# Kernel optimization log

Measured on AMD Instinct MI355X. Metric: run time of the kernel, lower is better.

## Reference

```python
import jax, jax.numpy as jnp
import numpy as np

N, L, C, NHEAD = 4, 2048, 1024, 8
D = C // NHEAD
EPS_ATTN = 1e-6
EPS_LN = 1e-5


def _w(key, shape, scale=0.02):
    return jax.random.normal(key, shape, dtype=jnp.float32) * scale


def setup_inputs() -> dict:
    key = jax.random.key(0)
    ks = jax.random.split(key, 32)
    inp = {
        'depth_feat': jax.random.normal(ks[0], (N, L, C), dtype=jnp.float32),
        'context_feat': jax.random.normal(ks[1], (N, L, C), dtype=jnp.float32),
        'depth_pos': jax.random.normal(ks[2], (N, L, C), dtype=jnp.float32),
        # encoder params (weights stored [in, out]; y = x @ W)
        'e_wq': _w(ks[3], (C, C)), 'e_wk': _w(ks[4], (C, C)), 'e_wv': _w(ks[5], (C, C)),
        'e_wm': _w(ks[6], (C, C)),
        'e_w1': _w(ks[7], (C, 2 * C)), 'e_w2': _w(ks[8], (2 * C, C)),
        'e_g1': jnp.ones((C,), jnp.float32), 'e_b1': jnp.zeros((C,), jnp.float32),
        'e_g2': jnp.ones((C,), jnp.float32), 'e_b2': jnp.zeros((C,), jnp.float32),
        # decoder params
        'd_wq0': _w(ks[9], (C, C)), 'd_wk0': _w(ks[10], (C, C)), 'd_wv0': _w(ks[11], (C, C)),
        'd_wm0': _w(ks[12], (C, C)),
        'd_wq1': _w(ks[13], (C, C)), 'd_wk1': _w(ks[14], (C, C)), 'd_wv1': _w(ks[15], (C, C)),
        'd_wm1': _w(ks[16], (C, C)),
        'd_w1': _w(ks[17], (C, 2 * C)), 'd_w2': _w(ks[18], (2 * C, C)),
        'd_g0': jnp.ones((C,), jnp.float32), 'd_b0': jnp.zeros((C,), jnp.float32),
        'd_g1': jnp.ones((C,), jnp.float32), 'd_b1': jnp.zeros((C,), jnp.float32),
        'd_g2': jnp.ones((C,), jnp.float32), 'd_b2': jnp.zeros((C,), jnp.float32),
    }
    return inp


def layernorm(x, g, b):
    m = jnp.mean(x, axis=-1, keepdims=True)
    v = jnp.mean(jnp.square(x - m), axis=-1, keepdims=True)
    return (x - m) * jax.lax.rsqrt(v + EPS_LN) * g + b


def linear_attention(q, k, v):
    # q,k,v: [N, L, H, D]; elu+1 feature map, O(L) kernelized attention
    Q = jax.nn.elu(q) + 1.0
    K = jax.nn.elu(k) + 1.0
    vlen = v.shape[1]
    v = v / vlen
    KV = jnp.einsum('nshd,nshv->nhdv', K, v)                    # [N,H,D,D]
    Z = 1.0 / (jnp.einsum('nlhd,nhd->nlh', Q, K.sum(axis=1)) + EPS_ATTN)
    out = jnp.einsum('nlhd,nhdv,nlh->nlhv', Q, KV, Z) * vlen    # [N,L,H,D]
    return out


def heads(x):
    n, l, c = x.shape
    return x.reshape(n, l, NHEAD, D)


def encoder_layer(x, wq, wk, wv, wm, w1, w2, g1, b1, g2, b2):
    n, l, c = x.shape
    msg = linear_attention(heads(x @ wq), heads(x @ wk), heads(x @ wv))
    msg = msg.reshape(n, l, c) @ wm
    x = x + layernorm(msg, g1, b1)
    x = x + layernorm(jax.nn.relu(x @ w1) @ w2, g2, b2)
    return x


def decoder_layer(x, src, wq0, wk0, wv0, wm0, wq1, wk1, wv1, wm1, w1, w2, g0, b0, g1, b1, g2, b2):
    n, l, c = x.shape
    msg = linear_attention(heads(x @ wq0), heads(x @ wk0), heads(x @ wv0))
    msg = msg.reshape(n, l, c) @ wm0
    x = x + layernorm(msg, g0, b0)
    msg = linear_attention(heads(x @ wq1), heads(src @ wk1), heads(src @ wv1))
    msg = msg.reshape(n, l, c) @ wm1
    x = x + layernorm(msg, g1, b1)
    x = x + layernorm(jax.nn.relu(x @ w1) @ w2, g2, b2)
    return x


def reference(depth_feat, context_feat, depth_pos,
              e_wq, e_wk, e_wv, e_wm, e_w1, e_w2, e_g1, e_b1, e_g2, e_b2,
              d_wq0, d_wk0, d_wv0, d_wm0, d_wq1, d_wk1, d_wv1, d_wm1,
              d_w1, d_w2, d_g0, d_b0, d_g1, d_b1, d_g2, d_b2):
    ctx = context_feat + depth_pos
    ctx = encoder_layer(ctx, e_wq, e_wk, e_wv, e_wm, e_w1, e_w2, e_g1, e_b1, e_g2, e_b2)
    out = decoder_layer(depth_feat, ctx,
                        d_wq0, d_wk0, d_wv0, d_wm0,
                        d_wq1, d_wk1, d_wv1, d_wm1,
                        d_w1, d_w2, d_g0, d_b0, d_g1, d_b1, d_g2, d_b2)
    return out
```

## Files before the change

### kernel.cpp

```cpp
#include <hip/hip_runtime.h>
#include <cstdint>

#define N_B 4
#define L_S 2048
#define C_F 1024
#define H_N 8
#define D_H 128
#define M_T (N_B * L_S)

typedef __bf16 bf16;
typedef __bf16 bf16x4 __attribute__((ext_vector_type(4)));
typedef __bf16 bf16x8 __attribute__((ext_vector_type(8)));
typedef float f32x4 __attribute__((ext_vector_type(4)));

typedef __attribute__((address_space(1))) void gvoid_t;
typedef __attribute__((address_space(3))) void lvoid_t;

__device__ __forceinline__ void lds_cp16(void* lds, const void* g) {
    __builtin_amdgcn_global_load_lds((gvoid_t*)g, (lvoid_t*)lds, 16, 0, 0);
}

__device__ __forceinline__ float elup1(float x) {
    return x > 0.0f ? x + 1.0f : __expf(x);
}

__device__ __forceinline__ void load4f(const void* base, size_t e0, int isbf, float* o) {
    if (isbf) {
        bf16x4 v = *(const bf16x4*)((const bf16*)base + e0);
        o[0] = (float)v[0]; o[1] = (float)v[1]; o[2] = (float)v[2]; o[3] = (float)v[3];
    } else {
        float4 v = *(const float4*)((const float*)base + e0);
        o[0] = v.x; o[1] = v.y; o[2] = v.z; o[3] = v.w;
    }
}

__global__ void detect_dtype(const unsigned int* g1, int* flag) {
    if (threadIdx.x == 0 && blockIdx.x == 0)
        *flag = (g1[0] == 0x3F803F80u) ? 1 : 0;
}

__global__ __launch_bounds__(256) void transpose_any(
        const void* __restrict__ src, bf16* __restrict__ dst,
        int R, int Cc, const int* __restrict__ flagp) {
    const int isbf = *flagp;
    __shared__ bf16 tile[32][33];
    const int bx = blockIdx.x * 32;
    const int by = blockIdx.y * 32;
    const int tx = threadIdx.x & 31;
    const int ty = threadIdx.x >> 5;
#pragma unroll
    for (int i = 0; i < 32; i += 8) {
        size_t ix = (size_t)(by + ty + i) * Cc + bx + tx;
        float v = isbf ? (float)((const bf16*)src)[ix] : ((const float*)src)[ix];
        tile[ty + i][tx] = (bf16)v;
    }
    __syncthreads();
#pragma unroll
    for (int i = 0; i < 32; i += 8)
        dst[(size_t)(bx + ty + i) * R + by + tx] = tile[tx][ty + i];
}

struct TAll {
    const void* src[16];
    unsigned int dstoff[16];
    int R[16];
    int C[16];
    int tile0[17];
};

__global__ __launch_bounds__(256) void transpose_all(
        TAll p, bf16* __restrict__ twall, const int* __restrict__ flagp) {
    const int isbf = *flagp;
    int gid = blockIdx.x;
    int w = 0;
    while (gid >= p.tile0[w + 1]) ++w;
    const int local = gid - p.tile0[w];
    const int R = p.R[w], Cc = p.C[w];
    const int tilesx = Cc >> 5;
    const int bx = (local % tilesx) * 32;
    const int by = (local / tilesx) * 32;
    const void* src = p.src[w];
    bf16* dst = twall + p.dstoff[w];
    __shared__ bf16 tile[32][33];
    const int tx = threadIdx.x & 31;
    const int ty = threadIdx.x >> 5;
#pragma unroll
    for (int i = 0; i < 32; i += 8) {
        size_t ix = (size_t)(by + ty + i) * Cc + bx + tx;
        float v = isbf ? (float)((const bf16*)src)[ix] : ((const float*)src)[ix];
        tile[ty + i][tx] = (bf16)v;
    }
    __syncthreads();
#pragma unroll
    for (int i = 0; i < 32; i += 8)
        dst[(size_t)(bx + ty + i) * R + by + tx] = tile[tx][ty + i];
}

template <int ACT>
__global__ __launch_bounds__(256, 2) void gemm_bt(
        const bf16* __restrict__ A, const bf16* __restrict__ Bt,
        bf16* __restrict__ C, int M, int N, int K) {
    __shared__ bf16 sA[128 * 64];
    __shared__ bf16 sB[128 * 64];
    const int t = threadIdx.x;
    const int lane = t & 63;
    const int w = t >> 6;
    const int wm = (w >> 1) * 64, wn = (w & 1) * 64;
    const int lr = lane & 15, lq = lane >> 4;
    const int m0 = blockIdx.y * 128, n0 = blockIdx.x * 128;

    f32x4 acc[4][4] = {};

    for (int kt = 0; kt < K; kt += 64) {
        const bf16* Ag = A + (size_t)m0 * K + kt;
        const bf16* Bg = Bt + (size_t)n0 * K + kt;
#pragma unroll
        for (int i = 0; i < 4; ++i) {
            int ci = t + i * 256;
            int r = ci >> 3, c8 = (ci & 7) * 8;
            lds_cp16(&sA[ci * 8], Ag + (size_t)r * K + c8);
        }
#pragma unroll
        for (int i = 0; i < 4; ++i) {
            int ci = t + i * 256;
            int r = ci >> 3, c8 = (ci & 7) * 8;
            lds_cp16(&sB[ci * 8], Bg + (size_t)r * K + c8);
        }
        __syncthreads();
#pragma unroll
        for (int kk = 0; kk < 64; kk += 32) {
            bf16x8 af[4], bfr[4];
#pragma unroll
            for (int mi = 0; mi < 4; ++mi)
                af[mi] = *(const bf16x8*)&sA[(wm + mi * 16 + lr) * 64 + kk + lq * 8];
#pragma unroll
            for (int ni = 0; ni < 4; ++ni)
                bfr[ni] = *(const bf16x8*)&sB[(wn + ni * 16 + lr) * 64 + kk + lq * 8];
#pragma unroll
            for (int mi = 0; mi < 4; ++mi)
#pragma unroll
                for (int ni = 0; ni < 4; ++ni)
                    acc[mi][ni] = __builtin_amdgcn_mfma_f32_16x16x32_bf16(
                        af[mi], bfr[ni], acc[mi][ni], 0, 0, 0);
        }
        __syncthreads();
    }
#pragma unroll
    for (int mi = 0; mi < 4; ++mi)
#pragma unroll
        for (int ni = 0; ni < 4; ++ni)
#pragma unroll
            for (int r = 0; r < 4; ++r) {
                int row = m0 + wm + mi * 16 + lq * 4 + r;
                int col = n0 + wn + ni * 16 + lr;
                float v = acc[mi][ni][r];
                if (ACT == 1) v = fmaxf(v, 0.0f);
                if (ACT == 2) v = v > 0.0f ? v + 1.0f : __expf(v);
                C[(size_t)row * N + col] = (bf16)v;
            }
}

__global__ __launch_bounds__(256, 2) void attn_kv_mfma(
        const bf16* __restrict__ ktg, const bf16* __restrict__ vtg,
        bf16* __restrict__ KVp, float* __restrict__ KSp) {
    const int nh = blockIdx.x;
    const int chunk = blockIdx.y;
    const int n = nh >> 3, h = nh & 7;
    const int t = threadIdx.x;
    const int lane = t & 63;
    const int w = t >> 6;
    const int wm = (w >> 1) * 64, wn = (w & 1) * 64;
    const int lr = lane & 15, lq = lane >> 4;
    __shared__ bf16 sA[128 * 64];
    __shared__ bf16 sB[128 * 64];
    const size_t base = (size_t)(h * D_H) * M_T + (size_t)n * L_S + chunk * 128;

    f32x4 acc[4][4] = {};
    float ks = 0.0f;
    const int dh = t >> 1, half = (t & 1) * 32;

    for (int kt = 0; kt < 128; kt += 64) {
        const bf16* Ag = vtg + base + kt;
        const bf16* Bg = ktg + base + kt;
#pragma unroll
        for (int i = 0; i < 4; ++i) {
            int ci = t + i * 256;
            int r = ci >> 3, c8 = (ci & 7) * 8;
            lds_cp16(&sA[ci * 8], Ag + (size_t)r * M_T + c8);
        }
#pragma unroll
        for (int i = 0; i < 4; ++i) {
            int ci = t + i * 256;
            int r = ci >> 3, c8 = (ci & 7) * 8;
            lds_cp16(&sB[ci * 8], Bg + (size_t)r * M_T + c8);
        }
        __syncthreads();
#pragma unroll
        for (int j = 0; j < 4; ++j) {
            bf16x8 v = *(const bf16x8*)&sB[dh * 64 + half + j * 8];
#pragma unroll
            for (int m = 0; m < 8; ++m) ks += (float)v[m];
        }
#pragma unroll
        for (int kk = 0; kk < 64; kk += 32) {
            bf16x8 af[4], bfr[4];
#pragma unroll
            for (int mi = 0; mi < 4; ++mi)
                af[mi] = *(const bf16x8*)&sA[(wm + mi * 16 + lr) * 64 + kk + lq * 8];
#pragma unroll
            for (int ni = 0; ni < 4; ++ni)
                bfr[ni] = *(const bf16x8*)&sB[(wn + ni * 16 + lr) * 64 + kk + lq * 8];
#pragma unroll
            for (int mi = 0; mi < 4; ++mi)
#pragma unroll
                for (int ni = 0; ni < 4; ++ni)
                    acc[mi][ni] = __builtin_amdgcn_mfma_f32_16x16x32_bf16(
                        af[mi], bfr[ni], acc[mi][ni], 0, 0, 0);
        }
        __syncthreads();
    }
    float ko = __shfl_xor(ks, 1);
    if (!(t & 1)) KSp[(nh * 16 + chunk) * D_H + dh] = ks + ko;

    bf16* out = KVp + ((size_t)(nh * 16 + chunk)) * (D_H * D_H);
#pragma unroll
    for (int mi = 0; mi < 4; ++mi)
#pragma unroll
        for (int ni = 0; ni < 4; ++ni)
#pragma unroll
            for (int r = 0; r < 4; ++r) {
                int row = wm + mi * 16 + lq * 4 + r;
                int col = wn + ni * 16 + lr;
                out[(size_t)row * D_H + col] = (bf16)acc[mi][ni][r];
            }
}

__global__ __launch_bounds__(256) void attn_reduce_t(
        const bf16* __restrict__ KVp, const float* __restrict__ KSp,
        bf16* __restrict__ KVt, float* __restrict__ Ksum) {
    const int nh = blockIdx.x;
    const int es = blockIdx.y;
    const int t = threadIdx.x;
    const size_t base = (size_t)nh * 16 * (D_H * D_H) + es * 4096 + t * 16;
    float fa[16] = {};
    for (int c = 0; c < 16; ++c) {
        const bf16* p = KVp + base + (size_t)c * (D_H * D_H);
        bf16x8 a = *(const bf16x8*)p;
        bf16x8 b = *(const bf16x8*)(p + 8);
#pragma unroll
        for (int m = 0; m < 8; ++m) { fa[m] += (float)a[m]; fa[8 + m] += (float)b[m]; }
    }
    bf16* o = KVt + (size_t)nh * (D_H * D_H) + es * 4096 + t * 16;
    bf16x8 oa, ob;
#pragma unroll
    for (int m = 0; m < 8; ++m) { oa[m] = (bf16)fa[m]; ob[m] = (bf16)fa[8 + m]; }
    *(bf16x8*)o = oa;
    *(bf16x8*)(o + 8) = ob;
    if (es == 0 && t < 128) {
        float s = 0.0f;
#pragma unroll
        for (int c = 0; c < 16; ++c) s += KSp[(nh * 16 + c) * D_H + t];
        Ksum[nh * D_H + t] = s;
    }
}

__global__ __launch_bounds__(256, 2) void attn_out_mfma(
        const bf16* __restrict__ qb, const bf16* __restrict__ KVt,
        const float* __restrict__ Ksum, bf16* __restrict__ ab) {
    const int nh = blockIdx.x, tile = blockIdx.y;
    const int n = nh >> 3, h = nh & 7;
    const int t = threadIdx.x;
    const int lane = t & 63;
    const int w = t >> 6;
    const int wm = (w >> 1) * 64, wn = (w & 1) * 64;
    const int lr = lane & 15, lq = lane >> 4;
    __shared__ bf16 sA[128 * 64];
    __shared__ bf16 sB[128 * 64];
    __shared__ float sKs[128];
    __shared__ float sZp[128][2];
    __shared__ float sZ[128];
    if (t < 128) sKs[t] = Ksum[nh * D_H + t];

    f32x4 acc[4][4] = {};
    float zacc = 0.0f;
    const int zrow = t >> 1, zoff = (t & 1) * 32;
    const size_t qbase = ((size_t)(n * L_S + tile * 128)) * C_F + h * D_H;

    for (int kt = 0; kt < 128; kt += 64) {
        __syncthreads();
#pragma unroll
        for (int i = 0; i < 4; ++i) {
            int ci = t + i * 256;
            int r = ci >> 3, c8 = (ci & 7) * 8;
            lds_cp16(&sA[ci * 8], qb + qbase + (size_t)r * C_F + kt + c8);
            lds_cp16(&sB[ci * 8], KVt + (size_t)nh * (D_H * D_H) + (size_t)r * D_H + kt + c8);
        }
        __syncthreads();
#pragma unroll 8
        for (int j = 0; j < 32; ++j)
            zacc += (float)sA[zrow * 64 + zoff + j] * sKs[kt + zoff + j];
#pragma unroll
        for (int kk = 0; kk < 64; kk += 32) {
            bf16x8 af[4], bfr[4];
#pragma unroll
            for (int mi = 0; mi < 4; ++mi)
                af[mi] = *(const bf16x8*)&sA[(wm + mi * 16 + lr) * 64 + kk + lq * 8];
#pragma unroll
            for (int ni = 0; ni < 4; ++ni)
                bfr[ni] = *(const bf16x8*)&sB[(wn + ni * 16 + lr) * 64 + kk + lq * 8];
#pragma unroll
            for (int mi = 0; mi < 4; ++mi)
#pragma unroll
                for (int ni = 0; ni < 4; ++ni)
                    acc[mi][ni] = __builtin_amdgcn_mfma_f32_16x16x32_bf16(
                        af[mi], bfr[ni], acc[mi][ni], 0, 0, 0);
        }
    }
    sZp[zrow][t & 1] = zacc;
    __syncthreads();
    if (t < 128) sZ[t] = 1.0f / (sZp[t][0] + sZp[t][1] + 1e-6f);
    __syncthreads();
#pragma unroll
    for (int mi = 0; mi < 4; ++mi)
#pragma unroll
        for (int ni = 0; ni < 4; ++ni)
#pragma unroll
            for (int r = 0; r < 4; ++r) {
                int row = wm + mi * 16 + lq * 4 + r;
                int col = wn + ni * 16 + lr;
                ab[qbase + (size_t)row * C_F + col] = (bf16)(acc[mi][ni][r] * sZ[row]);
            }
}

template <int F32OUT>
__global__ __launch_bounds__(256) void ln_res(
        const bf16* __restrict__ msg, const void* __restrict__ g,
        const void* __restrict__ bb, const int* __restrict__ flagp,
        const bf16* __restrict__ xin, void* __restrict__ xout) {
    const int isbf = *flagp;
    const int row = blockIdx.x * 4 + (threadIdx.x >> 6);
    const int lane = threadIdx.x & 63;
    const size_t base = (size_t)row * C_F;
    float m[16];
#pragma unroll
    for (int k = 0; k < 4; ++k) {
        bf16x4 v = *(const bf16x4*)(msg + base + k * 256 + lane * 4);
        m[k * 4 + 0] = (float)v[0]; m[k * 4 + 1] = (float)v[1];
        m[k * 4 + 2] = (float)v[2]; m[k * 4 + 3] = (float)v[3];
    }
    float s1 = 0.0f, s2 = 0.0f;
#pragma unroll
    for (int q = 0; q < 16; ++q) { s1 += m[q]; s2 += m[q] * m[q]; }
#pragma unroll
    for (int off = 32; off > 0; off >>= 1) {
        s1 += __shfl_down(s1, off);
        s2 += __shfl_down(s2, off);
    }
    s1 = __shfl(s1, 0);
    s2 = __shfl(s2, 0);
    const float mean = s1 / C_F;
    const float rs = rsqrtf(s2 / C_F - mean * mean + 1e-5f);
#pragma unroll
    for (int k = 0; k < 4; ++k) {
        const size_t cix = k * 256 + lane * 4;
        float ga[4], ba[4];
        load4f(g, cix, isbf, ga);
        load4f(bb, cix, isbf, ba);
        bf16x4 x4 = *(const bf16x4*)(xin + base + cix);
        if (F32OUT) {
            float4 of;
            of.x = (float)x4[0] + (m[k * 4 + 0] - mean) * rs * ga[0] + ba[0];
            of.y = (float)x4[1] + (m[k * 4 + 1] - mean) * rs * ga[1] + ba[1];
            of.z = (float)x4[2] + (m[k * 4 + 2] - mean) * rs * ga[2] + ba[2];
            of.w = (float)x4[3] + (m[k * 4 + 3] - mean) * rs * ga[3] + ba[3];
            *(float4*)((float*)xout + base + cix) = of;
        } else {
            bf16x4 ob;
            ob[0] = (bf16)((float)x4[0] + (m[k * 4 + 0] - mean) * rs * ga[0] + ba[0]);
            ob[1] = (bf16)((float)x4[1] + (m[k * 4 + 1] - mean) * rs * ga[1] + ba[1]);
            ob[2] = (bf16)((float)x4[2] + (m[k * 4 + 2] - mean) * rs * ga[2] + ba[2]);
            ob[3] = (bf16)((float)x4[3] + (m[k * 4 + 3] - mean) * rs * ga[3] + ba[3]);
            *(bf16x4*)((bf16*)xout + base + cix) = ob;
        }
    }
}

__global__ __launch_bounds__(256) void init_ctx_kernel(
        const void* __restrict__ a, const void* __restrict__ b,
        const int* __restrict__ flagp, bf16* __restrict__ xb) {
    const int isbf = *flagp;
    const size_t i = ((size_t)blockIdx.x * 256 + threadIdx.x) * 4;
    float av[4], bv[4];
    load4f(a, i, isbf, av);
    load4f(b, i, isbf, bv);
    bf16x4 o;
#pragma unroll
    for (int q = 0; q < 4; ++q) o[q] = (bf16)(av[q] + bv[q]);
    *(bf16x4*)(xb + i) = o;
}

__global__ __launch_bounds__(256) void conv_copy_kernel(
        const void* __restrict__ a, const int* __restrict__ flagp,
        bf16* __restrict__ xb) {
    const int isbf = *flagp;
    const size_t i = ((size_t)blockIdx.x * 256 + threadIdx.x) * 4;
    float av[4];
    load4f(a, i, isbf, av);
    bf16x4 o;
#pragma unroll
    for (int q = 0; q < 4; ++q) o[q] = (bf16)av[q];
    *(bf16x4*)(xb + i) = o;
}

extern "C" void kernel_launch(void* const* d_in, const int* in_sizes, int n_in,
                              void* d_out, int out_size, void* d_ws, size_t ws_size,
                              hipStream_t stream) {
    const size_t MB = 1u << 20;
    uint8_t* W = (uint8_t*)d_ws;
    bf16* xb    = (bf16*)(W + 0);
    bf16* ctxb  = (bf16*)(W + 16 * MB);
    bf16* qb    = (bf16*)(W + 32 * MB);
    bf16* kb    = (bf16*)(W + 48 * MB);
    bf16* vb    = (bf16*)(W + 64 * MB);
    bf16* hb    = kb;
    bf16* S     = (bf16*)(W + 80 * MB);
    bf16* TW    = (bf16*)(W + 96 * MB);
    bf16* KVp   = S;
    float* KSp  = (float*)(W + 100 * MB);
    bf16* KVt   = (bf16*)(W + 101 * MB);
    float* Ksum = (float*)(W + 102 * MB);
    int*   flag = (int*)(W + 102 * MB + 64 * 1024);
    bf16* TWall = (bf16*)(W + 104 * MB);
    const bool batched = (ws_size >= 145 * MB);

    detect_dtype<<<1, 64, 0, stream>>>((const unsigned int*)d_in[9], flag);

    const int widx[16] = {3,4,5,6,7,8,13,14,15,16,17,18,19,20,21,22};
    const int wR[16]   = {1024,1024,1024,1024,1024,2048,1024,1024,1024,1024,
                          1024,1024,1024,1024,1024,2048};
    const int wC[16]   = {1024,1024,1024,1024,2048,1024,1024,1024,1024,1024,
                          1024,1024,1024,1024,2048,1024};
    unsigned int off[16];
    if (batched) {
        TAll p;
        unsigned int acc = 0;
        int tacc = 0;
        for (int i = 0; i < 16; ++i) {
            p.src[i] = d_in[widx[i]];
            p.dstoff[i] = acc;
            p.R[i] = wR[i];
            p.C[i] = wC[i];
            p.tile0[i] = tacc;
            off[i] = acc;
            acc += (unsigned int)wR[i] * wC[i];
            tacc += (wR[i] / 32) * (wC[i] / 32);
        }
        p.tile0[16] = tacc;
        transpose_all<<<tacc, 256, 0, stream>>>(p, TWall, flag);
    }
    auto BT = [&](int idx) -> const bf16* {
        int s = 0;
        for (int i = 0; i < 16; ++i) if (widx[i] == idx) { s = i; break; }
        if (batched) return TWall + off[s];
        dim3 g(wC[s] / 32, wR[s] / 32);
        transpose_any<<<g, 256, 0, stream>>>(d_in[idx], TW, wR[s], wC[s], flag);
        return TW;
    };
    auto TG = [&](int idx, const bf16* A, bf16* Cc, int Nn, int Kk, int act) {
        const bf16* Bt = BT(idx);
        dim3 g(Nn / 128, M_T / 128);
        if (act == 1)      gemm_bt<1><<<g, 256, 0, stream>>>(A, Bt, Cc, M_T, Nn, Kk);
        else if (act == 2) gemm_bt<2><<<g, 256, 0, stream>>>(A, Bt, Cc, M_T, Nn, Kk);
        else               gemm_bt<0><<<g, 256, 0, stream>>>(A, Bt, Cc, M_T, Nn, Kk);
    };
    auto TGT = [&](int idx, const bf16* X, bf16* Ct, int act) {
        const bf16* Wt = BT(idx);
        dim3 g(M_T / 128, C_F / 128);
        if (act == 2) gemm_bt<2><<<g, 256, 0, stream>>>(Wt, X, Ct, C_F, M_T, C_F);
        else          gemm_bt<0><<<g, 256, 0, stream>>>(Wt, X, Ct, C_F, M_T, C_F);
    };
    auto ATT = [&](const bf16* q, const bf16* k, const bf16* v, bf16* o) {
        attn_kv_mfma<<<dim3(32, 16), 256, 0, stream>>>(k, v, KVp, KSp);
        attn_reduce_t<<<dim3(32, 4), 256, 0, stream>>>(KVp, KSp, KVt, Ksum);
        attn_out_mfma<<<dim3(32, 16), 256, 0, stream>>>(q, KVt, Ksum, o);
    };
    auto LN = [&](const bf16* m, int gi, int bi, const bf16* xi, bf16* xo) {
        ln_res<0><<<M_T / 4, 256, 0, stream>>>(m, d_in[gi], d_in[bi], flag, xi, (void*)xo);
    };

    init_ctx_kernel<<<M_T * C_F / 1024, 256, 0, stream>>>(d_in[1], d_in[2], flag, xb);
    TG(3, xb, qb, C_F, C_F, 2);
    TGT(4, xb, kb, 2);
    TGT(5, xb, vb, 0);
    ATT(qb, kb, vb, S);
    TG(6, S, qb, C_F, C_F, 0);
    LN(qb, 9, 10, xb, xb);
    TG(7, xb, hb, 2 * C_F, C_F, 1);
    TG(8, hb, S, C_F, 2 * C_F, 0);
    LN(S, 11, 12, xb, ctxb);

    conv_copy_kernel<<<M_T * C_F / 1024, 256, 0, stream>>>(d_in[0], flag, xb);
    TG(13, xb, qb, C_F, C_F, 2);
    TGT(14, xb, kb, 2);
    TGT(15, xb, vb, 0);
    ATT(qb, kb, vb, S);
    TG(16, S, qb, C_F, C_F, 0);
    LN(qb, 23, 24, xb, xb);
    TG(17, xb, qb, C_F, C_F, 2);
    TGT(18, ctxb, kb, 2);
    TGT(19, ctxb, vb, 0);
    ATT(qb, kb, vb, S);
    TG(20, S, qb, C_F, C_F, 0);
    LN(qb, 25, 26, xb, xb);
    TG(21, xb, hb, 2 * C_F, C_F, 1);
    TG(22, hb, S, C_F, 2 * C_F, 0);
    ln_res<1><<<M_T / 4, 256, 0, stream>>>(S, d_in[27], d_in[28], flag, xb, d_out);
}
```

Measured before the change: 933.1 us.

## Add 256x256 pipelined GEMM and fuse K/V projections into one launch

```diff
diff --git a/kernel.cpp b/kernel.cpp
--- a/kernel.cpp
+++ b/kernel.cpp
@@ -156,6 +156,104 @@
                 float v = acc[mi][ni][r];
                 if (ACT == 1) v = fmaxf(v, 0.0f);
                 if (ACT == 2) v = v > 0.0f ? v + 1.0f : __expf(v);
+                C[(size_t)row * N + col] = (bf16)v;
+            }
+}
+
+#define STAGE_T(sarr, Gbase, ldstride, Tt)                                    \
+    {                                                                         \
+        const int sl_ = (Tt) & 3;                                             \
+        _Pragma("unroll")                                                     \
+        for (int i_ = 0; i_ < 2; ++i_) {                                      \
+            int ci_ = t + i_ * 512;                                           \
+            int r_ = ci_ >> 2, c8_ = (ci_ & 3) * 8;                           \
+            lds_cp16(&sarr[sl_ * 8192 + ci_ * 8],                             \
+                     (Gbase) + (size_t)r_ * (ldstride) + ((Tt) << 5) +        \
+                         (c8_ ^ ((r_ & 3) << 3)));                            \
+        }                                                                     \
+    }
+
+template <int ACT>
+__global__ __launch_bounds__(512, 2) void gemm256(
+        const bf16* __restrict__ A, const bf16* __restrict__ Bt,
+        bf16* __restrict__ C, int M, int N, int K, int actsplit) {
+    __shared__ bf16 sA[4 * 256 * 32];
+    __shared__ bf16 sB[4 * 256 * 32];
+    const int t = threadIdx.x;
+    const int lane = t & 63;
+    const int w = t >> 6;
+    const int wr = w >> 2, wc = w & 3;
+    const int lr = lane & 15, lq = lane >> 4;
+    const int m0 = blockIdx.y * 256, n0 = blockIdx.x * 256;
+    const int nt = K >> 5;
+
+    const bf16* Ab = A + (size_t)m0 * K;
+    const bf16* Bb = Bt + (size_t)n0 * K;
+
+    f32x4 acc[8][4] = {};
+
+    STAGE_T(sA, Ab, K, 0); STAGE_T(sB, Bb, K, 0);
+    STAGE_T(sA, Ab, K, 1); STAGE_T(sB, Bb, K, 1);
+    asm volatile("s_waitcnt vmcnt(4)" ::: "memory");
+    __builtin_amdgcn_s_barrier();
+
+    for (int T = 0; T < nt; ++T) {
+        const bf16* sAs = &sA[(T & 3) * 8192];
+        const bf16* sBs = &sB[(T & 3) * 8192];
+        bf16x8 af[4], bfr[4], ag[4];
+#pragma unroll
+        for (int mi = 0; mi < 4; ++mi) {
+            int row = wr * 128 + mi * 16 + lr;
+            af[mi] = *(const bf16x8*)&sAs[row * 32 + ((lq * 8) ^ ((row & 3) << 3))];
+        }
+#pragma unroll
+        for (int ni = 0; ni < 4; ++ni) {
+            int row = wc * 64 + ni * 16 + lr;
+            bfr[ni] = *(const bf16x8*)&sBs[row * 32 + ((lq * 8) ^ ((row & 3) << 3))];
+        }
+        if (T + 2 < nt) STAGE_T(sA, Ab, K, T + 2);
+        __builtin_amdgcn_s_barrier();
+        __builtin_amdgcn_s_setprio(1);
+#pragma unroll
+        for (int mi = 0; mi < 4; ++mi)
+#pragma unroll
+            for (int ni = 0; ni < 4; ++ni)
+                acc[mi][ni] = __builtin_amdgcn_mfma_f32_16x16x32_bf16(
+                    af[mi], bfr[ni], acc[mi][ni], 0, 0, 0);
+        __builtin_amdgcn_s_setprio(0);
+        __builtin_amdgcn_s_barrier();
+#pragma unroll
+        for (int mi = 0; mi < 4; ++mi) {
+            int row = wr * 128 + (mi + 4) * 16 + lr;
+            ag[mi] = *(const bf16x8*)&sAs[row * 32 + ((lq * 8) ^ ((row & 3) << 3))];
+        }
+        if (T + 2 < nt) STAGE_T(sB, Bb, K, T + 2);
+        __builtin_amdgcn_s_barrier();
+        __builtin_amdgcn_s_setprio(1);
+#pragma unroll
+        for (int mi = 0; mi < 4; ++mi)
+#pragma unroll
+            for (int ni = 0; ni < 4; ++ni)
+                acc[mi + 4][ni] = __builtin_amdgcn_mfma_f32_16x16x32_bf16(
+                    ag[mi], bfr[ni], acc[mi + 4][ni], 0, 0, 0);
+        __builtin_amdgcn_s_setprio(0);
+        if (T + 1 < nt) {
+            if (T + 2 < nt) asm volatile("s_waitcnt vmcnt(4)" ::: "memory");
+            else            asm volatile("s_waitcnt vmcnt(0)" ::: "memory");
+        }
+        __builtin_amdgcn_s_barrier();
+    }
+#pragma unroll
+    for (int mi = 0; mi < 8; ++mi)
+#pragma unroll
+        for (int ni = 0; ni < 4; ++ni)
+#pragma unroll
+            for (int r = 0; r < 4; ++r) {
+                int row = m0 + wr * 128 + mi * 16 + lq * 4 + r;
+                int col = n0 + wc * 64 + ni * 16 + lr;
+                float v = acc[mi][ni][r];
+                if (ACT == 1) v = fmaxf(v, 0.0f);
+                if (ACT == 3 && row < actsplit) v = v > 0.0f ? v + 1.0f : __expf(v);
                 C[(size_t)row * N + col] = (bf16)v;
             }
 }
@@ -441,26 +539,30 @@
     const int wC[16]   = {1024,1024,1024,1024,2048,1024,1024,1024,1024,1024,
                           1024,1024,1024,1024,2048,1024};
     unsigned int off[16];
+    {
+        unsigned int acc = 0;
+        for (int i = 0; i < 16; ++i) { off[i] = acc; acc += (unsigned int)wR[i] * wC[i]; }
+    }
     if (batched) {
         TAll p;
-        unsigned int acc = 0;
         int tacc = 0;
         for (int i = 0; i < 16; ++i) {
             p.src[i] = d_in[widx[i]];
-            p.dstoff[i] = acc;
+            p.dstoff[i] = off[i];
             p.R[i] = wR[i];
             p.C[i] = wC[i];
             p.tile0[i] = tacc;
-            off[i] = acc;
-            acc += (unsigned int)wR[i] * wC[i];
             tacc += (wR[i] / 32) * (wC[i] / 32);
         }
         p.tile0[16] = tacc;
         transpose_all<<<tacc, 256, 0, stream>>>(p, TWall, flag);
     }
+    auto SLOT = [&](int idx) {
+        for (int i = 0; i < 16; ++i) if (widx[i] == idx) return i;
+        return 0;
+    };
     auto BT = [&](int idx) -> const bf16* {
-        int s = 0;
-        for (int i = 0; i < 16; ++i) if (widx[i] == idx) { s = i; break; }
+        int s = SLOT(idx);
         if (batched) return TWall + off[s];
         dim3 g(wC[s] / 32, wR[s] / 32);
         transpose_any<<<g, 256, 0, stream>>>(d_in[idx], TW, wR[s], wC[s], flag);
@@ -473,11 +575,23 @@
         else if (act == 2) gemm_bt<2><<<g, 256, 0, stream>>>(A, Bt, Cc, M_T, Nn, Kk);
         else               gemm_bt<0><<<g, 256, 0, stream>>>(A, Bt, Cc, M_T, Nn, Kk);
     };
-    auto TGT = [&](int idx, const bf16* X, bf16* Ct, int act) {
-        const bf16* Wt = BT(idx);
-        dim3 g(M_T / 128, C_F / 128);
-        if (act == 2) gemm_bt<2><<<g, 256, 0, stream>>>(Wt, X, Ct, C_F, M_T, C_F);
-        else          gemm_bt<0><<<g, 256, 0, stream>>>(Wt, X, Ct, C_F, M_T, C_F);
+    auto KVF = [&](int kidx, int vidx, const bf16* X) {
+        const bf16* Wt;
+        if (batched) {
+            Wt = TWall + off[SLOT(kidx)];
+        } else {
+            dim3 g(32, 32);
+            transpose_any<<<g, 256, 0, stream>>>(d_in[kidx], TW, 1024, 1024, flag);
+            transpose_any<<<g, 256, 0, stream>>>(d_in[vidx], TW + 1024 * 1024, 1024, 1024, flag);
+            Wt = TW;
+        }
+        dim3 g(M_T / 256, (2 * C_F) / 256);
+        gemm256<3><<<g, 512, 0, stream>>>(Wt, X, kb, 2 * C_F, M_T, C_F, C_F);
+    };
+    auto FFN1 = [&](int idx, const bf16* A) {
+        const bf16* Bt = BT(idx);
+        dim3 g((2 * C_F) / 256, M_T / 256);
+        gemm256<1><<<g, 512, 0, stream>>>(A, Bt, hb, M_T, 2 * C_F, C_F, 0);
     };
     auto ATT = [&](const bf16* q, const bf16* k, const bf16* v, bf16* o) {
         attn_kv_mfma<<<dim3(32, 16), 256, 0, stream>>>(k, v, KVp, KSp);
@@ -490,29 +604,26 @@
 
     init_ctx_kernel<<<M_T * C_F / 1024, 256, 0, stream>>>(d_in[1], d_in[2], flag, xb);
     TG(3, xb, qb, C_F, C_F, 2);
-    TGT(4, xb, kb, 2);
-    TGT(5, xb, vb, 0);
+    KVF(4, 5, xb);
     ATT(qb, kb, vb, S);
     TG(6, S, qb, C_F, C_F, 0);
     LN(qb, 9, 10, xb, xb);
-    TG(7, xb, hb, 2 * C_F, C_F, 1);
+    FFN1(7, xb);
     TG(8, hb, S, C_F, 2 * C_F, 0);
     LN(S, 11, 12, xb, ctxb);
 
     conv_copy_kernel<<<M_T * C_F / 1024, 256, 0, stream>>>(d_in[0], flag, xb);
     TG(13, xb, qb, C_F, C_F, 2);
-    TGT(14, xb, kb, 2);
-    TGT(15, xb, vb, 0);
+    KVF(14, 15, xb);
     ATT(qb, kb, vb, S);
     TG(16, S, qb, C_F, C_F, 0);
     LN(qb, 23, 24, xb, xb);
     TG(17, xb, qb, C_F, C_F, 2);
-    TGT(18, ctxb, kb, 2);
-    TGT(19, ctxb, vb, 0);
+    KVF(18, 19, ctxb);
     ATT(qb, kb, vb, S);
     TG(20, S, qb, C_F, C_F, 0);
     LN(qb, 25, 26, xb, xb);
-    TG(21, xb, hb, 2 * C_F, C_F, 1);
+    FFN1(21, xb);
     TG(22, hb, S, C_F, 2 * C_F, 0);
     ln_res<1><<<M_T / 4, 256, 0, stream>>>(S, d_in[27], d_in[28], flag, xb, d_out);
 }
```

Measured after the change: 867.3 us. -7.1%, faster.
